# Performance work log

Hardware: AMD Instinct MI355X
Metric: run time of the kernel (lower is better)

## Reference

```python
import jax, jax.numpy as jnp
import numpy as np


def setup_inputs() -> dict:
    key = jax.random.key(0)
    k1, k2, k3, k4 = jax.random.split(key, 4)
    B, N, dim, heads, dim_head = 4, 1025, 768, 12, 64
    inner = heads * dim_head
    x = jax.random.normal(k1, (B, N, dim), dtype=jnp.float32)
    # binary occlusion mask over the N-1 patch tokens (CLS handled inside forward)
    mask = (jax.random.uniform(k2, (B, N - 1, dim)) > 0.5).astype(jnp.float32)
    w_qkv = jax.random.normal(k3, (inner * 3, dim), dtype=jnp.float32) * 0.02
    w_out = jax.random.normal(k4, (dim, inner), dtype=jnp.float32) * 0.02
    b_out = jnp.zeros((dim,), dtype=jnp.float32)
    return {"x": x, "mask": mask, "w_qkv": w_qkv, "w_out": w_out, "b_out": b_out, "heads": heads}


def reference(x, mask, w_qkv, w_out, b_out, heads):
    B, N, dim = x.shape
    inner = w_qkv.shape[0] // 3
    d = inner // heads
    scale = d ** -0.5

    def split_heads(t):  # [B, n, h*d] -> [B, h, n, d]
        return t.reshape(B, t.shape[1], heads, d).transpose(0, 2, 1, 3)

    qkv = x @ w_qkv.T  # [B, N, 3*inner]
    q, k, v = map(split_heads, jnp.split(qkv, 3, axis=-1))

    # --- mask propagation (torch.no_grad block) ---
    mask_sg = jax.lax.stop_gradient(mask)
    qkv_m = mask_sg @ jax.lax.stop_gradient(jnp.abs(w_qkv)).T  # [B, N-1, 3*inner]

    def norm_mask(t):
        t = split_heads(t)  # [B, h, N-1, d]
        t = t / (1e-6 + jnp.max(t, axis=2, keepdims=True))
        return jnp.concatenate([jnp.ones_like(t[:, :, :1]), t], axis=2)  # [B, h, N, d]

    q_m, k_m, v_m = map(norm_mask, jnp.split(qkv_m, 3, axis=-1))
    updated = (jnp.mean(mask_sg, axis=-1, keepdims=True) > 0.0).astype(x.dtype)  # [B, N-1, 1]
    updated = jnp.concatenate([jnp.ones_like(updated[:, :1]), updated], axis=1)  # [B, N, 1]

    # --- masked attention ---
    dots = jnp.einsum('bhnd,bhmd->bhnm', q * q_m, k * k_m) * scale
    attn = jax.nn.softmax(dots, axis=-1)
    out = jnp.einsum('bhnm,bhmd->bhnd', attn, v_m * v)
    out = out.transpose(0, 2, 1, 3).reshape(B, N, inner) * updated
    out = out @ w_out.T + b_out

    # --- mask output propagation (no grad) ---
    m = jax.lax.stop_gradient(jnp.einsum('bhnm,bhmd->bhnd', attn, v_m))
    m = m.transpose(0, 2, 1, 3).reshape(B, N, inner) * updated
    m = m @ jax.lax.stop_gradient(jnp.abs(w_out)).T
    return (out, m[:, 1:])
```

## Files before the change

kernel.cpp:

```cpp
#include <hip/hip_runtime.h>
#include <cmath>

#define TPB 256
#define ATPB 128

static const int NTOK  = 1025;
static const int DIM   = 768;
static const int HEADS = 12;
static const int QK3   = 2304;
static const int ROWS  = 4 * NTOK;
static const int MROWS = 4 * (NTOK - 1);
static const int MPAD  = 4224;
static const int NPAD  = 1088;
static const int VROWS = 129;
static const size_t OUT0 = (size_t)ROWS * DIM;
static const size_t APLANE = (size_t)MPAD * DIM;

static const size_t OFF_QKV16  = 0;
static const size_t OFF_QKVM16 = 4800000;
static const size_t OFF_QE     = 9600000;
static const size_t OFF_KE     = 11300000;
static const size_t OFF_VT     = 13000000;
static const size_t OFF_ABF    = 16400000;
static const size_t OFF_WQ     = 19700000;
static const size_t OFF_WO     = 21500000;
static const size_t OFF_CMAX   = 22100000;
static const size_t OFF_UPD    = 22110000;

typedef __attribute__((ext_vector_type(8))) short short8;
typedef __attribute__((ext_vector_type(4))) float f32x4;

__device__ __forceinline__ unsigned short f2bf(float f) {
    union { float f; unsigned int u; } c; c.f = f;
    unsigned int u = c.u + 0x7fffu + ((c.u >> 16) & 1u);
    return (unsigned short)(u >> 16);
}
__device__ __forceinline__ float bf2f(unsigned short u) {
    union { unsigned int u; float f; } c; c.u = (unsigned int)u << 16;
    return c.f;
}
__device__ __forceinline__ void gl_lds16(const unsigned short* g, unsigned short* l) {
    __builtin_amdgcn_global_load_lds(
        (const __attribute__((address_space(1))) unsigned int*)g,
        (__attribute__((address_space(3))) unsigned int*)l, 16, 0, 0);
}

__global__ __launch_bounds__(TPB)
void k_cvt(const float* __restrict__ x, const float* __restrict__ mask,
           const float* __restrict__ wqkv, const float* __restrict__ wout,
           unsigned short* __restrict__ Abf, unsigned short* __restrict__ Wq,
           unsigned short* __restrict__ Wo)
{
    const int z = blockIdx.z;
    const size_t idx = ((size_t)blockIdx.x * TPB + threadIdx.x) * 8;
    unsigned short o[8] __attribute__((aligned(16)));
    if (z <= 1) {
        if (idx >= APLANE) return;
        const int row = (int)(idx / DIM);
        const int M = z ? MROWS : ROWS;
        const float* src = z ? mask : x;
        if (row < M) {
            float a[8];
            *(float4*)&a[0] = *(const float4*)(src + idx);
            *(float4*)&a[4] = *(const float4*)(src + idx + 4);
#pragma unroll
            for (int i = 0; i < 8; ++i) o[i] = f2bf(a[i]);
        } else {
#pragma unroll
            for (int i = 0; i < 8; ++i) o[i] = 0;
        }
        *(short8*)(Abf + (size_t)z * APLANE + idx) = *(short8*)o;
    } else {
        const size_t tot = (z == 2) ? (size_t)QK3 * DIM : (size_t)DIM * DIM;
        if (idx >= tot) return;
        const float* src = (z == 2) ? wqkv : wout;
        unsigned short* dst = (z == 2) ? Wq : Wo;
        float a[8];
        *(float4*)&a[0] = *(const float4*)(src + idx);
        *(float4*)&a[4] = *(const float4*)(src + idx + 4);
        unsigned short oa[8] __attribute__((aligned(16)));
#pragma unroll
        for (int i = 0; i < 8; ++i) { o[i] = f2bf(a[i]); oa[i] = f2bf(fabsf(a[i])); }
        *(short8*)(dst + idx) = *(short8*)o;
        *(short8*)(dst + tot + idx) = *(short8*)oa;
    }
}

__global__ __launch_bounds__(TPB)
void k_gemm_qkv_mfma(const unsigned short* __restrict__ Abf,
                     const unsigned short* __restrict__ Wq,
                     unsigned short* __restrict__ qkv16,
                     unsigned short* __restrict__ qkvm16,
                     float* __restrict__ cmax)
{
    const int z = blockIdx.z;
    const int rowT = blockIdx.y * 128, colT = blockIdx.x * 128;
    if (z == 1 && rowT >= MROWS) return;
    const unsigned short* A = Abf + (size_t)z * APLANE;
    const unsigned short* B = Wq + (size_t)z * QK3 * DIM;

    __shared__ unsigned short As[128 * 64];
    __shared__ unsigned short Bs[128 * 64];

    const int t = threadIdx.x;
    const int w = t >> 6, lane = t & 63, l15 = lane & 15, quad = lane >> 4;
    const int wm = (w & 1) * 64, wn = (w >> 1) * 64;
    const int sr = t >> 2, sk = (t & 3) * 8;

    f32x4 acc[4][4];
#pragma unroll
    for (int i = 0; i < 4; ++i)
#pragma unroll
        for (int j = 0; j < 4; ++j) acc[i][j] = (f32x4){0.f, 0.f, 0.f, 0.f};

    for (int k0 = 0; k0 < DIM; k0 += 64) {
        __syncthreads();
#pragma unroll
        for (int c = 0; c < 4; ++c) {
            const int gr = sr + (c & 1) * 64;
            const int gk = k0 + (c >> 1) * 32 + sk;
            gl_lds16(A + (size_t)(rowT + gr) * DIM + gk, As + c * 2048 + t * 8);
            gl_lds16(B + (size_t)(colT + gr) * DIM + gk, Bs + c * 2048 + t * 8);
        }
        __syncthreads();
        short8 fa[2][4], fb[2][4];
#pragma unroll
        for (int kk = 0; kk < 2; ++kk) {
#pragma unroll
            for (int mi = 0; mi < 4; ++mi)
                fa[kk][mi] = *(const short8*)(As + kk * 4096 + (wm + mi * 16 + l15) * 32 + quad * 8);
#pragma unroll
            for (int ni = 0; ni < 4; ++ni)
                fb[kk][ni] = *(const short8*)(Bs + kk * 4096 + (wn + ni * 16 + l15) * 32 + quad * 8);
        }
#pragma unroll
        for (int kk = 0; kk < 2; ++kk)
#pragma unroll
            for (int mi = 0; mi < 4; ++mi)
#pragma unroll
                for (int ni = 0; ni < 4; ++ni)
                    acc[mi][ni] = __builtin_amdgcn_mfma_f32_16x16x32_bf16(fa[kk][mi], fb[kk][ni], acc[mi][ni], 0, 0, 0);
    }

    float cm[4] = {0.f, 0.f, 0.f, 0.f};
#pragma unroll
    for (int mi = 0; mi < 4; ++mi)
#pragma unroll
        for (int ni = 0; ni < 4; ++ni) {
            const int col = colT + wn + ni * 16 + l15;
#pragma unroll
            for (int r = 0; r < 4; ++r) {
                const int row = rowT + wm + mi * 16 + quad * 4 + r;
                const float v = acc[mi][ni][r];
                if (z == 0) {
                    if (row < ROWS) qkv16[(size_t)row * QK3 + col] = f2bf(v);
                } else {
                    qkvm16[(size_t)row * QK3 + col] = f2bf(v);
                    cm[ni] = fmaxf(cm[ni], v);
                }
            }
        }
    if (z == 1) {
        const int bb = rowT >> 10;
#pragma unroll
        for (int ni = 0; ni < 4; ++ni) {
            float m = cm[ni];
            m = fmaxf(m, __shfl_xor(m, 16, 64));
            m = fmaxf(m, __shfl_xor(m, 32, 64));
            if (quad == 0)
                atomicMax((int*)&cmax[bb * QK3 + colT + wn + ni * 16 + l15], __float_as_int(m));
        }
    }
}

__global__ __launch_bounds__(TPB)
void k_misc(const float* __restrict__ mask, float* __restrict__ upd,
            unsigned short* __restrict__ vt)
{
    const int bx = blockIdx.x;
    if (bx >= 1025) {
        const int bh = bx - 1025;
        unsigned short* p = vt + ((size_t)bh * VROWS + 128) * NPAD;
        for (int n = threadIdx.x; n < NPAD; n += TPB)
            p[n] = (n < NTOK) ? (unsigned short)0x3F80 : (unsigned short)0;
        return;
    }
    const int w = threadIdx.x >> 6, lane = threadIdx.x & 63;
    const int r = bx * 4 + w;
    if (r >= ROWS) return;
    const int b = r / NTOK, n = r % NTOK;
    float res = 1.f;
    if (n > 0) {
        const float* p = mask + (size_t)(b * (NTOK - 1) + (n - 1)) * DIM;
        float s = 0.f;
        for (int i = lane; i < DIM; i += 64) s += p[i];
#pragma unroll
        for (int off = 32; off > 0; off >>= 1) s += __shfl_xor(s, off, 64);
        res = (s > 0.f) ? 1.f : 0.f;
    }
    if (lane == 0) upd[r] = res;
}

__global__ __launch_bounds__(TPB)
void k_prep(const unsigned short* __restrict__ qkv16,
            const unsigned short* __restrict__ qkvm16,
            const float* __restrict__ cmax, unsigned short* __restrict__ qe,
            unsigned short* __restrict__ ke, unsigned short* __restrict__ vt)
{
    __shared__ unsigned short Vt_l[128 * 66];
    const int t = threadIdx.x;
    const int nt = blockIdx.x, h = blockIdx.y, b = blockIdx.z;
    const int bh = b * HEADS + h;
    const int nl = t >> 2, ds0 = (t & 3) * 16;
    const int n = nt * 64 + nl;
    const bool valid = n < NTOK;
    const int col0 = h * 64 + ds0;

    unsigned short q16[16] __attribute__((aligned(16))) = {0};
    unsigned short k16[16] __attribute__((aligned(16))) = {0};
    unsigned short v16[16] __attribute__((aligned(16))) = {0};
    unsigned short qm16[16] __attribute__((aligned(16)));
    unsigned short km16[16] __attribute__((aligned(16)));
    unsigned short vm16[16] __attribute__((aligned(16)));
    float cq[16], ck[16], cv[16];

    const bool useM = valid && (n > 0);
    if (valid) {
        const size_t br = (size_t)(b * NTOK + n) * QK3 + col0;
        *(short8*)&q16[0] = *(const short8*)(qkv16 + br);
        *(short8*)&q16[8] = *(const short8*)(qkv16 + br + 8);
        *(short8*)&k16[0] = *(const short8*)(qkv16 + br + 768);
        *(short8*)&k16[8] = *(const short8*)(qkv16 + br + 776);
        *(short8*)&v16[0] = *(const short8*)(qkv16 + br + 1536);
        *(short8*)&v16[8] = *(const short8*)(qkv16 + br + 1544);
    }
    if (useM) {
        const size_t mr = (size_t)(b * 1024 + (n - 1)) * QK3 + col0;
        *(short8*)&qm16[0] = *(const short8*)(qkvm16 + mr);
        *(short8*)&qm16[8] = *(const short8*)(qkvm16 + mr + 8);
        *(short8*)&km16[0] = *(const short8*)(qkvm16 + mr + 768);
        *(short8*)&km16[8] = *(const short8*)(qkvm16 + mr + 776);
        *(short8*)&vm16[0] = *(const short8*)(qkvm16 + mr + 1536);
        *(short8*)&vm16[8] = *(const short8*)(qkvm16 + mr + 1544);
        const int cb = b * QK3 + col0;
#pragma unroll
        for (int i = 0; i < 4; ++i) {
            *(float4*)&cq[i * 4] = *(const float4*)(cmax + cb + i * 4);
            *(float4*)&ck[i * 4] = *(const float4*)(cmax + cb + 768 + i * 4);
            *(float4*)&cv[i * 4] = *(const float4*)(cmax + cb + 1536 + i * 4);
        }
    }

    unsigned short oq[16] __attribute__((aligned(16)));
    unsigned short ok[16] __attribute__((aligned(16)));
#pragma unroll
    for (int idx = 0; idx < 16; ++idx) {
        const float qm = useM ? bf2f(qm16[idx]) / (1e-6f + cq[idx]) : 1.f;
        const float km = useM ? bf2f(km16[idx]) / (1e-6f + ck[idx]) : 1.f;
        const float vm = valid ? (useM ? bf2f(vm16[idx]) / (1e-6f + cv[idx]) : 1.f) : 0.f;
        oq[idx] = f2bf(bf2f(q16[idx]) * qm * 0.125f);
        ok[idx] = f2bf(bf2f(k16[idx]) * km);
        const int d = ds0 + idx;
        Vt_l[d * 66 + nl]        = f2bf(bf2f(v16[idx]) * vm);
        Vt_l[(64 + d) * 66 + nl] = f2bf(vm);
    }
    if (valid) {
        unsigned short* qp = qe + ((size_t)bh * NPAD + n) * 64 + ds0;
        unsigned short* kp = ke + ((size_t)bh * NPAD + n) * 64 + ds0;
        *(short8*)qp       = *(short8*)oq;
        *(short8*)(qp + 8) = *(short8*)(oq + 8);
        *(short8*)kp       = *(short8*)ok;
        *(short8*)(kp + 8) = *(short8*)(ok + 8);
    }
    __syncthreads();
    const int c = t >> 1, nh = (t & 1) * 32;
    unsigned short ov[32] __attribute__((aligned(16)));
#pragma unroll
    for (int i = 0; i < 32; ++i) ov[i] = Vt_l[c * 66 + nh + i];
    unsigned short* vp = vt + ((size_t)bh * VROWS + c) * NPAD + nt * 64 + nh;
#pragma unroll
    for (int i = 0; i < 4; ++i) *(short8*)(vp + i * 8) = *(short8*)(ov + i * 8);
}

__global__ __launch_bounds__(ATPB)
void k_attn(const unsigned short* __restrict__ qe, const unsigned short* __restrict__ ke,
            const unsigned short* __restrict__ vt, const float* __restrict__ upd,
            unsigned short* __restrict__ ab2)
{
    __shared__ short8 KsF[8 * 64];
    __shared__ short8 VsF[18 * 64];

    const int t = threadIdx.x;
    const int w = t >> 6, lane = t & 63;
    const int l15 = lane & 15, quad = lane >> 4;
    const int bh = blockIdx.y;
    const int b = bh / HEADS, h = bh % HEADS;
    const int q0 = blockIdx.x * 64;

    short8 qf[2][2];
#pragma unroll
    for (int j = 0; j < 2; ++j) {
        const unsigned short* qp = qe + ((size_t)bh * NPAD + q0 + w * 32 + j * 16 + l15) * 64 + (quad << 3);
        qf[j][0] = *(const short8*)qp;
        qf[j][1] = *(const short8*)(qp + 32);
    }
    const int pA = (quad & 1) * 32 + l15;
    const int pB = pA + 16;
    const bool lo32 = (lane < 32);

    f32x4 acc[2][9];
#pragma unroll
    for (int j = 0; j < 2; ++j)
#pragma unroll
        for (int g = 0; g < 9; ++g) acc[j][g] = (f32x4){0.f, 0.f, 0.f, 0.f};

    for (int kt = 0; kt < 17; ++kt) {
        const int kn0 = kt * 64;
        __syncthreads();
#pragma unroll
        for (int gi = 0; gi < 4; ++gi) {
            const int g = 4 * w + gi, kk = g >> 2, nc = g & 3;
            const unsigned short* gp = ke + ((size_t)bh * NPAD + kn0 + nc * 16 + l15) * 64
                                          + kk * 32 + (quad << 3);
            gl_lds16(gp, (unsigned short*)&KsF[g * 64] + lane * 8);
        }
#pragma unroll
        for (int i = 0; i < 9; ++i) {
            const int g = w + 2 * i;
            const int kk = (g >= 9) ? 1 : 0, c8 = g - kk * 9;
            const unsigned short* gp = vt + ((size_t)bh * VROWS + c8 * 16 + l15) * NPAD
                                          + kn0 + kk * 32 + (quad << 3);
            gl_lds16(gp, (unsigned short*)&VsF[g * 64] + lane * 8);
        }
        __syncthreads();

        f32x4 s[2][4];
#pragma unroll
        for (int nc = 0; nc < 4; ++nc) {
            const short8 k0 = KsF[nc * 64 + lane];
            const short8 k1 = KsF[(4 + nc) * 64 + lane];
#pragma unroll
            for (int j = 0; j < 2; ++j) {
                f32x4 z = (f32x4){0.f, 0.f, 0.f, 0.f};
                z = __builtin_amdgcn_mfma_f32_16x16x32_bf16(k0, qf[j][0], z, 0, 0, 0);
                z = __builtin_amdgcn_mfma_f32_16x16x32_bf16(k1, qf[j][1], z, 0, 0, 0);
                s[j][nc] = z;
            }
        }
        short8 pf[2][2];
#pragma unroll
        for (int j = 0; j < 2; ++j) {
            unsigned int dA[4], dB[4];
#pragma unroll
            for (int nc = 0; nc < 4; ++nc) {
                const float p0 = __expf(s[j][nc][0] - 10.f);
                const float p1 = __expf(s[j][nc][1] - 10.f);
                const float p2 = __expf(s[j][nc][2] - 10.f);
                const float p3 = __expf(s[j][nc][3] - 10.f);
                dA[nc] = (unsigned int)f2bf(p0) | ((unsigned int)f2bf(p1) << 16);
                dB[nc] = (unsigned int)f2bf(p2) | ((unsigned int)f2bf(p3) << 16);
            }
            union { int i[4]; short8 s; } u0, u1;
            {
                const int a0 = __shfl((int)dA[0], pA, 64), a1 = __shfl((int)dA[1], pA, 64);
                const int b0 = __shfl((int)dB[0], pA, 64), b1 = __shfl((int)dB[1], pA, 64);
                const int a2 = __shfl((int)dA[0], pB, 64), a3 = __shfl((int)dA[1], pB, 64);
                const int b2 = __shfl((int)dB[0], pB, 64), b3 = __shfl((int)dB[1], pB, 64);
                u0.i[0] = lo32 ? a0 : a1;
                u0.i[1] = lo32 ? b0 : b1;
                u0.i[2] = lo32 ? a2 : a3;
                u0.i[3] = lo32 ? b2 : b3;
            }
            {
                const int a0 = __shfl((int)dA[2], pA, 64), a1 = __shfl((int)dA[3], pA, 64);
                const int b0 = __shfl((int)dB[2], pA, 64), b1 = __shfl((int)dB[3], pA, 64);
                const int a2 = __shfl((int)dA[2], pB, 64), a3 = __shfl((int)dA[3], pB, 64);
                const int b2 = __shfl((int)dB[2], pB, 64), b3 = __shfl((int)dB[3], pB, 64);
                u1.i[0] = lo32 ? a0 : a1;
                u1.i[1] = lo32 ? b0 : b1;
                u1.i[2] = lo32 ? a2 : a3;
                u1.i[3] = lo32 ? b2 : b3;
            }
            pf[j][0] = u0.s;
            pf[j][1] = u1.s;
        }
#pragma unroll
        for (int g = 0; g < 9; ++g) {
            const short8 v0 = VsF[g * 64 + lane];
            const short8 v1 = VsF[(9 + g) * 64 + lane];
#pragma unroll
            for (int j = 0; j < 2; ++j) {
                acc[j][g] = __builtin_amdgcn_mfma_f32_16x16x32_bf16(v0, pf[j][0], acc[j][g], 0, 0, 0);
                acc[j][g] = __builtin_amdgcn_mfma_f32_16x16x32_bf16(v1, pf[j][1], acc[j][g], 0, 0, 0);
            }
        }
    }

#pragma unroll
    for (int j = 0; j < 2; ++j) {
        const float lq = __shfl(acc[j][8][0], l15, 64);
        const int qrow = q0 + w * 32 + j * 16 + l15;
        if (qrow < NTOK) {
            const size_t rg = (size_t)b * NTOK + qrow;
            const float inv = upd[rg] / lq;
#pragma unroll
            for (int g = 0; g < 8; ++g) {
                uint2 pk;
                pk.x = (unsigned int)f2bf(acc[j][g][0] * inv) | ((unsigned int)f2bf(acc[j][g][1] * inv) << 16);
                pk.y = (unsigned int)f2bf(acc[j][g][2] * inv) | ((unsigned int)f2bf(acc[j][g][3] * inv) << 16);
                const size_t addr = (size_t)(g >> 2) * APLANE + rg * DIM + h * 64 + (g & 3) * 16 + quad * 4;
                *(uint2*)(ab2 + addr) = pk;
            }
        }
    }
}

__global__ __launch_bounds__(TPB)
void k_gemm_out_mfma(const unsigned short* __restrict__ ab2,
                     const unsigned short* __restrict__ Wo,
                     const float* __restrict__ bout, float* __restrict__ dout)
{
    const int z = blockIdx.z;
    const unsigned short* A = ab2 + (size_t)z * APLANE;
    const unsigned short* B = Wo + (size_t)z * DIM * DIM;

    __shared__ unsigned short As[128 * 32];
    __shared__ unsigned short Bs[128 * 32];

    const int t = threadIdx.x;
    const int w = t >> 6, lane = t & 63, l15 = lane & 15, quad = lane >> 4;
    const int rowT = blockIdx.y * 128, colT = blockIdx.x * 128;
    const int wm = (w & 1) * 64, wn = (w >> 1) * 64;

    const int r0 = t >> 2, kc = (t & 3) * 8;
    const unsigned short* Ap = A + (size_t)(rowT + r0) * DIM + kc;
    const unsigned short* Bp = B + (size_t)(colT + r0) * DIM + kc;

    f32x4 acc[4][4];
#pragma unroll
    for (int i = 0; i < 4; ++i)
#pragma unroll
        for (int j = 0; j < 4; ++j) acc[i][j] = (f32x4){0.f, 0.f, 0.f, 0.f};

    for (int k0 = 0; k0 < DIM; k0 += 32) {
        __syncthreads();
        gl_lds16(Ap + k0,            As + t * 8);
        gl_lds16(Ap + 64 * DIM + k0, As + (t + 256) * 8);
        gl_lds16(Bp + k0,            Bs + t * 8);
        gl_lds16(Bp + 64 * DIM + k0, Bs + (t + 256) * 8);
        __syncthreads();
        short8 fa[4], fb[4];
#pragma unroll
        for (int mi = 0; mi < 4; ++mi)
            fa[mi] = *(const short8*)(As + (wm + mi * 16 + l15) * 32 + quad * 8);
#pragma unroll
        for (int ni = 0; ni < 4; ++ni)
            fb[ni] = *(const short8*)(Bs + (wn + ni * 16 + l15) * 32 + quad * 8);
#pragma unroll
        for (int mi = 0; mi < 4; ++mi)
#pragma unroll
            for (int ni = 0; ni < 4; ++ni)
                acc[mi][ni] = __builtin_amdgcn_mfma_f32_16x16x32_bf16(fa[mi], fb[ni], acc[mi][ni], 0, 0, 0);
    }
#pragma unroll
    for (int mi = 0; mi < 4; ++mi)
#pragma unroll
        for (int ni = 0; ni < 4; ++ni) {
            const int col = colT + wn + ni * 16 + l15;
            const float bb = (z == 0) ? bout[col] : 0.f;
#pragma unroll
            for (int r = 0; r < 4; ++r) {
                const int row = rowT + wm + mi * 16 + quad * 4 + r;
                if (row >= ROWS) continue;
                const int b = row / NTOK, n = row % NTOK;
                if (z == 0) {
                    dout[(size_t)row * DIM + col] = acc[mi][ni][r] + bb;
                } else if (n >= 1) {
                    dout[OUT0 + ((size_t)(b * (NTOK - 1) + (n - 1))) * DIM + col] = acc[mi][ni][r];
                }
            }
        }
}

extern "C" void kernel_launch(void* const* d_in, const int* in_sizes, int n_in,
                              void* d_out, int out_size, void* d_ws, size_t ws_size,
                              hipStream_t stream)
{
    const float* x    = (const float*)d_in[0];
    const float* mask = (const float*)d_in[1];
    const float* wqkv = (const float*)d_in[2];
    const float* wout = (const float*)d_in[3];
    const float* bout = (const float*)d_in[4];
    float* ws = (float*)d_ws;
    unsigned short* qkv16  = (unsigned short*)(ws + OFF_QKV16);
    unsigned short* qkvm16 = (unsigned short*)(ws + OFF_QKVM16);
    unsigned short* qe  = (unsigned short*)(ws + OFF_QE);
    unsigned short* ke  = (unsigned short*)(ws + OFF_KE);
    unsigned short* vt  = (unsigned short*)(ws + OFF_VT);
    unsigned short* abf = (unsigned short*)(ws + OFF_ABF);
    unsigned short* wq  = (unsigned short*)(ws + OFF_WQ);
    unsigned short* wo  = (unsigned short*)(ws + OFF_WO);
    float* cmax = ws + OFF_CMAX;
    float* upd  = ws + OFF_UPD;
    float* out  = (float*)d_out;

    hipMemsetAsync(cmax, 0, 9216 * sizeof(float), stream);
    hipLaunchKernelGGL(k_cvt,           dim3(1584, 1, 4), dim3(TPB), 0, stream, x, mask, wqkv, wout, abf, wq, wo);
    hipLaunchKernelGGL(k_gemm_qkv_mfma, dim3(18, 33, 2),  dim3(TPB), 0, stream, abf, wq, qkv16, qkvm16, cmax);
    hipLaunchKernelGGL(k_misc,          dim3(1073),       dim3(TPB), 0, stream, mask, upd, vt);
    hipLaunchKernelGGL(k_prep,          dim3(17, 12, 4),  dim3(TPB), 0, stream, qkv16, qkvm16, cmax, qe, ke, vt);
    hipLaunchKernelGGL(k_attn,          dim3(17, 48),     dim3(ATPB), 0, stream, qe, ke, vt, upd, abf);
    hipLaunchKernelGGL(k_gemm_out_mfma, dim3(6, 33, 2),   dim3(TPB), 0, stream, abf, wo, bout, out);
}
```

Before: 249.0 us.

## Store K/V in MFMA fragment layout and load directly into registers in attention

The prep kernel now writes K and V directly in MFMA fragment order, so the attention kernel can load K/V tiles straight into registers instead of staging them through LDS behind barriers. Attention becomes one 64-thread wave per 32-query tile with a swizzled block order and register prefetch of the next K/V tile. The softmax denominator is now accumulated in registers rather than through an extra ones-row in V, which removes the 129th row and its memset pass. Exponentials switch to exp2 with log2e folded into the Q scale, bf16 packing uses v_cvt_pk_bf16_f32, and s_setprio is raised around the MFMA sections. In exchange the kernel carries more register pressure from the prefetched fragments, and LDS reuse of K/V across waves is lost.

```diff
diff --git a/kernel.cpp b/kernel.cpp
--- a/kernel.cpp
+++ b/kernel.cpp
@@ -2,7 +2,6 @@
 #include <cmath>
 
 #define TPB 256
-#define ATPB 128
 
 static const int NTOK  = 1025;
 static const int DIM   = 768;
@@ -12,15 +11,14 @@
 static const int MROWS = 4 * (NTOK - 1);
 static const int MPAD  = 4224;
 static const int NPAD  = 1088;
-static const int VROWS = 129;
 static const size_t OUT0 = (size_t)ROWS * DIM;
 static const size_t APLANE = (size_t)MPAD * DIM;
 
 static const size_t OFF_QKV16  = 0;
 static const size_t OFF_QKVM16 = 4800000;
 static const size_t OFF_QE     = 9600000;
-static const size_t OFF_KE     = 11300000;
-static const size_t OFF_VT     = 13000000;
+static const size_t OFF_KF     = 11300000;
+static const size_t OFF_VF     = 13000000;
 static const size_t OFF_ABF    = 16400000;
 static const size_t OFF_WQ     = 19700000;
 static const size_t OFF_WO     = 21500000;
@@ -38,6 +36,11 @@
 __device__ __forceinline__ float bf2f(unsigned short u) {
     union { unsigned int u; float f; } c; c.u = (unsigned int)u << 16;
     return c.f;
+}
+__device__ __forceinline__ unsigned int cvtpk(float a, float b) {
+    unsigned int r;
+    asm("v_cvt_pk_bf16_f32 %0, %1, %2" : "=v"(r) : "v"(a), "v"(b));
+    return r;
 }
 __device__ __forceinline__ void gl_lds16(const unsigned short* g, unsigned short* l) {
     __builtin_amdgcn_global_load_lds(
@@ -174,17 +177,9 @@
 }
 
 __global__ __launch_bounds__(TPB)
-void k_misc(const float* __restrict__ mask, float* __restrict__ upd,
-            unsigned short* __restrict__ vt)
+void k_misc(const float* __restrict__ mask, float* __restrict__ upd)
 {
     const int bx = blockIdx.x;
-    if (bx >= 1025) {
-        const int bh = bx - 1025;
-        unsigned short* p = vt + ((size_t)bh * VROWS + 128) * NPAD;
-        for (int n = threadIdx.x; n < NPAD; n += TPB)
-            p[n] = (n < NTOK) ? (unsigned short)0x3F80 : (unsigned short)0;
-        return;
-    }
     const int w = threadIdx.x >> 6, lane = threadIdx.x & 63;
     const int r = bx * 4 + w;
     if (r >= ROWS) return;
@@ -205,7 +200,7 @@
 void k_prep(const unsigned short* __restrict__ qkv16,
             const unsigned short* __restrict__ qkvm16,
             const float* __restrict__ cmax, unsigned short* __restrict__ qe,
-            unsigned short* __restrict__ ke, unsigned short* __restrict__ vt)
+            unsigned short* __restrict__ kfrag, unsigned short* __restrict__ vfrag)
 {
     __shared__ unsigned short Vt_l[128 * 66];
     const int t = threadIdx.x;
@@ -258,49 +253,53 @@
         const float qm = useM ? bf2f(qm16[idx]) / (1e-6f + cq[idx]) : 1.f;
         const float km = useM ? bf2f(km16[idx]) / (1e-6f + ck[idx]) : 1.f;
         const float vm = valid ? (useM ? bf2f(vm16[idx]) / (1e-6f + cv[idx]) : 1.f) : 0.f;
-        oq[idx] = f2bf(bf2f(q16[idx]) * qm * 0.125f);
+        oq[idx] = f2bf(bf2f(q16[idx]) * qm * 0.18033688f);
         ok[idx] = f2bf(bf2f(k16[idx]) * km);
         const int d = ds0 + idx;
         Vt_l[d * 66 + nl]        = f2bf(bf2f(v16[idx]) * vm);
         Vt_l[(64 + d) * 66 + nl] = f2bf(vm);
     }
-    if (valid) {
+    {
         unsigned short* qp = qe + ((size_t)bh * NPAD + n) * 64 + ds0;
-        unsigned short* kp = ke + ((size_t)bh * NPAD + n) * 64 + ds0;
         *(short8*)qp       = *(short8*)oq;
         *(short8*)(qp + 8) = *(short8*)(oq + 8);
-        *(short8*)kp       = *(short8*)ok;
-        *(short8*)(kp + 8) = *(short8*)(ok + 8);
+    }
+    {
+        const int nc = nl >> 4, l15 = nl & 15;
+        const int kk = ds0 >> 5, qb = (ds0 & 31) >> 3;
+        unsigned short* kp = kfrag + (((size_t)bh * 17 + nt) * 8 + kk * 4 + nc) * 512;
+        *(short8*)(kp + ((size_t)(qb * 16 + l15)) * 8)       = *(short8*)ok;
+        *(short8*)(kp + ((size_t)((qb + 1) * 16 + l15)) * 8) = *(short8*)(ok + 8);
     }
     __syncthreads();
     const int c = t >> 1, nh = (t & 1) * 32;
     unsigned short ov[32] __attribute__((aligned(16)));
 #pragma unroll
     for (int i = 0; i < 32; ++i) ov[i] = Vt_l[c * 66 + nh + i];
-    unsigned short* vp = vt + ((size_t)bh * VROWS + c) * NPAD + nt * 64 + nh;
-#pragma unroll
-    for (int i = 0; i < 4; ++i) *(short8*)(vp + i * 8) = *(short8*)(ov + i * 8);
-}
-
-__global__ __launch_bounds__(ATPB)
-void k_attn(const unsigned short* __restrict__ qe, const unsigned short* __restrict__ ke,
-            const unsigned short* __restrict__ vt, const float* __restrict__ upd,
+    const int c8 = c >> 4, l15v = c & 15, kkv = nh >> 5;
+    unsigned short* vp = vfrag + (((size_t)bh * 17 + nt) * 16 + c8 * 2 + kkv) * 512 + (size_t)l15v * 8;
+#pragma unroll
+    for (int qd = 0; qd < 4; ++qd)
+        *(short8*)(vp + (size_t)qd * 128) = *(short8*)(ov + qd * 8);
+}
+
+__global__ __launch_bounds__(64, 2)
+void k_attn(const unsigned short* __restrict__ qe, const unsigned short* __restrict__ kfrag,
+            const unsigned short* __restrict__ vfrag, const float* __restrict__ upd,
             unsigned short* __restrict__ ab2)
 {
-    __shared__ short8 KsF[8 * 64];
-    __shared__ short8 VsF[18 * 64];
-
-    const int t = threadIdx.x;
-    const int w = t >> 6, lane = t & 63;
+    const int flat = blockIdx.y * 33 + blockIdx.x;
+    const int d2 = (flat & 7) * 198 + (flat >> 3);
+    const int bh = d2 / 33, qt = d2 - bh * 33;
+    const int b = bh / HEADS, h = bh - b * HEADS;
+    const int lane = threadIdx.x;
     const int l15 = lane & 15, quad = lane >> 4;
-    const int bh = blockIdx.y;
-    const int b = bh / HEADS, h = bh % HEADS;
-    const int q0 = blockIdx.x * 64;
+    const int q0 = qt * 32;
 
     short8 qf[2][2];
 #pragma unroll
     for (int j = 0; j < 2; ++j) {
-        const unsigned short* qp = qe + ((size_t)bh * NPAD + q0 + w * 32 + j * 16 + l15) * 64 + (quad << 3);
+        const unsigned short* qp = qe + ((size_t)bh * NPAD + q0 + j * 16 + l15) * 64 + (quad << 3);
         qf[j][0] = *(const short8*)qp;
         qf[j][1] = *(const short8*)(qp + 32);
     }
@@ -308,58 +307,62 @@
     const int pB = pA + 16;
     const bool lo32 = (lane < 32);
 
-    f32x4 acc[2][9];
+    const unsigned short* kb = kfrag + (size_t)bh * (17 * 8 * 512) + (size_t)lane * 8;
+    const unsigned short* vb = vfrag + (size_t)bh * (17 * 16 * 512) + (size_t)lane * 8;
+
+    short8 kf[8], vf[16];
+#pragma unroll
+    for (int g = 0; g < 8; ++g) kf[g] = *(const short8*)(kb + g * 512);
+#pragma unroll
+    for (int g = 0; g < 16; ++g) vf[g] = *(const short8*)(vb + g * 512);
+
+    f32x4 acc[2][8];
+    float lac[2] = {0.f, 0.f};
 #pragma unroll
     for (int j = 0; j < 2; ++j)
 #pragma unroll
-        for (int g = 0; g < 9; ++g) acc[j][g] = (f32x4){0.f, 0.f, 0.f, 0.f};
-
+        for (int g = 0; g < 8; ++g) acc[j][g] = (f32x4){0.f, 0.f, 0.f, 0.f};
+
+    const float EC = 14.4269504f;
+
+#pragma clang loop unroll(disable)
     for (int kt = 0; kt < 17; ++kt) {
-        const int kn0 = kt * 64;
-        __syncthreads();
-#pragma unroll
-        for (int gi = 0; gi < 4; ++gi) {
-            const int g = 4 * w + gi, kk = g >> 2, nc = g & 3;
-            const unsigned short* gp = ke + ((size_t)bh * NPAD + kn0 + nc * 16 + l15) * 64
-                                          + kk * 32 + (quad << 3);
-            gl_lds16(gp, (unsigned short*)&KsF[g * 64] + lane * 8);
-        }
-#pragma unroll
-        for (int i = 0; i < 9; ++i) {
-            const int g = w + 2 * i;
-            const int kk = (g >= 9) ? 1 : 0, c8 = g - kk * 9;
-            const unsigned short* gp = vt + ((size_t)bh * VROWS + c8 * 16 + l15) * NPAD
-                                          + kn0 + kk * 32 + (quad << 3);
-            gl_lds16(gp, (unsigned short*)&VsF[g * 64] + lane * 8);
-        }
-        __syncthreads();
-
         f32x4 s[2][4];
+        __builtin_amdgcn_s_setprio(1);
 #pragma unroll
         for (int nc = 0; nc < 4; ++nc) {
-            const short8 k0 = KsF[nc * 64 + lane];
-            const short8 k1 = KsF[(4 + nc) * 64 + lane];
 #pragma unroll
             for (int j = 0; j < 2; ++j) {
                 f32x4 z = (f32x4){0.f, 0.f, 0.f, 0.f};
-                z = __builtin_amdgcn_mfma_f32_16x16x32_bf16(k0, qf[j][0], z, 0, 0, 0);
-                z = __builtin_amdgcn_mfma_f32_16x16x32_bf16(k1, qf[j][1], z, 0, 0, 0);
+                z = __builtin_amdgcn_mfma_f32_16x16x32_bf16(kf[nc], qf[j][0], z, 0, 0, 0);
+                z = __builtin_amdgcn_mfma_f32_16x16x32_bf16(kf[4 + nc], qf[j][1], z, 0, 0, 0);
                 s[j][nc] = z;
             }
+        }
+        __builtin_amdgcn_s_setprio(0);
+        if (kt < 16) {
+            const unsigned short* kn = kb + (size_t)(kt + 1) * 4096;
+#pragma unroll
+            for (int g = 0; g < 8; ++g) kf[g] = *(const short8*)(kn + g * 512);
         }
         short8 pf[2][2];
 #pragma unroll
         for (int j = 0; j < 2; ++j) {
             unsigned int dA[4], dB[4];
+            float psum = 0.f, p00 = 0.f;
 #pragma unroll
             for (int nc = 0; nc < 4; ++nc) {
-                const float p0 = __expf(s[j][nc][0] - 10.f);
-                const float p1 = __expf(s[j][nc][1] - 10.f);
-                const float p2 = __expf(s[j][nc][2] - 10.f);
-                const float p3 = __expf(s[j][nc][3] - 10.f);
-                dA[nc] = (unsigned int)f2bf(p0) | ((unsigned int)f2bf(p1) << 16);
-                dB[nc] = (unsigned int)f2bf(p2) | ((unsigned int)f2bf(p3) << 16);
-            }
+                const float p0 = __builtin_amdgcn_exp2f(s[j][nc][0] - EC);
+                const float p1 = __builtin_amdgcn_exp2f(s[j][nc][1] - EC);
+                const float p2 = __builtin_amdgcn_exp2f(s[j][nc][2] - EC);
+                const float p3 = __builtin_amdgcn_exp2f(s[j][nc][3] - EC);
+                dA[nc] = cvtpk(p0, p1);
+                dB[nc] = cvtpk(p2, p3);
+                psum += (p0 + p1) + (p2 + p3);
+                if (nc == 0) p00 = p0;
+            }
+            if (kt < 16) lac[j] += psum;
+            else if (quad == 0) lac[j] += p00;
             union { int i[4]; short8 s; } u0, u1;
             {
                 const int a0 = __shfl((int)dA[0], pA, 64), a1 = __shfl((int)dA[1], pA, 64);
@@ -384,30 +387,37 @@
             pf[j][0] = u0.s;
             pf[j][1] = u1.s;
         }
-#pragma unroll
-        for (int g = 0; g < 9; ++g) {
-            const short8 v0 = VsF[g * 64 + lane];
-            const short8 v1 = VsF[(9 + g) * 64 + lane];
+        __builtin_amdgcn_s_setprio(1);
+#pragma unroll
+        for (int g = 0; g < 8; ++g) {
 #pragma unroll
             for (int j = 0; j < 2; ++j) {
-                acc[j][g] = __builtin_amdgcn_mfma_f32_16x16x32_bf16(v0, pf[j][0], acc[j][g], 0, 0, 0);
-                acc[j][g] = __builtin_amdgcn_mfma_f32_16x16x32_bf16(v1, pf[j][1], acc[j][g], 0, 0, 0);
-            }
+                acc[j][g] = __builtin_amdgcn_mfma_f32_16x16x32_bf16(vf[2 * g],     pf[j][0], acc[j][g], 0, 0, 0);
+                acc[j][g] = __builtin_amdgcn_mfma_f32_16x16x32_bf16(vf[2 * g + 1], pf[j][1], acc[j][g], 0, 0, 0);
+            }
+        }
+        __builtin_amdgcn_s_setprio(0);
+        if (kt < 16) {
+            const unsigned short* vn = vb + (size_t)(kt + 1) * 8192;
+#pragma unroll
+            for (int g = 0; g < 16; ++g) vf[g] = *(const short8*)(vn + g * 512);
         }
     }
 
 #pragma unroll
     for (int j = 0; j < 2; ++j) {
-        const float lq = __shfl(acc[j][8][0], l15, 64);
-        const int qrow = q0 + w * 32 + j * 16 + l15;
+        float lq = lac[j];
+        lq += __shfl_xor(lq, 16, 64);
+        lq += __shfl_xor(lq, 32, 64);
+        const int qrow = q0 + j * 16 + l15;
         if (qrow < NTOK) {
             const size_t rg = (size_t)b * NTOK + qrow;
             const float inv = upd[rg] / lq;
 #pragma unroll
             for (int g = 0; g < 8; ++g) {
                 uint2 pk;
-                pk.x = (unsigned int)f2bf(acc[j][g][0] * inv) | ((unsigned int)f2bf(acc[j][g][1] * inv) << 16);
-                pk.y = (unsigned int)f2bf(acc[j][g][2] * inv) | ((unsigned int)f2bf(acc[j][g][3] * inv) << 16);
+                pk.x = cvtpk(acc[j][g][0] * inv, acc[j][g][1] * inv);
+                pk.y = cvtpk(acc[j][g][2] * inv, acc[j][g][3] * inv);
                 const size_t addr = (size_t)(g >> 2) * APLANE + rg * DIM + h * 64 + (g & 3) * 16 + quad * 4;
                 *(uint2*)(ab2 + addr) = pk;
             }
@@ -495,8 +505,8 @@
     unsigned short* qkv16  = (unsigned short*)(ws + OFF_QKV16);
     unsigned short* qkvm16 = (unsigned short*)(ws + OFF_QKVM16);
     unsigned short* qe  = (unsigned short*)(ws + OFF_QE);
-    unsigned short* ke  = (unsigned short*)(ws + OFF_KE);
-    unsigned short* vt  = (unsigned short*)(ws + OFF_VT);
+    unsigned short* kfr = (unsigned short*)(ws + OFF_KF);
+    unsigned short* vfr = (unsigned short*)(ws + OFF_VF);
     unsigned short* abf = (unsigned short*)(ws + OFF_ABF);
     unsigned short* wq  = (unsigned short*)(ws + OFF_WQ);
     unsigned short* wo  = (unsigned short*)(ws + OFF_WO);
@@ -507,8 +517,8 @@
     hipMemsetAsync(cmax, 0, 9216 * sizeof(float), stream);
     hipLaunchKernelGGL(k_cvt,           dim3(1584, 1, 4), dim3(TPB), 0, stream, x, mask, wqkv, wout, abf, wq, wo);
     hipLaunchKernelGGL(k_gemm_qkv_mfma, dim3(18, 33, 2),  dim3(TPB), 0, stream, abf, wq, qkv16, qkvm16, cmax);
-    hipLaunchKernelGGL(k_misc,          dim3(1073),       dim3(TPB), 0, stream, mask, upd, vt);
-    hipLaunchKernelGGL(k_prep,          dim3(17, 12, 4),  dim3(TPB), 0, stream, qkv16, qkvm16, cmax, qe, ke, vt);
-    hipLaunchKernelGGL(k_attn,          dim3(17, 48),     dim3(ATPB), 0, stream, qe, ke, vt, upd, abf);
+    hipLaunchKernelGGL(k_misc,          dim3(1025),       dim3(TPB), 0, stream, mask, upd);
+    hipLaunchKernelGGL(k_prep,          dim3(17, 12, 4),  dim3(TPB), 0, stream, qkv16, qkvm16, cmax, qe, kfr, vfr);
+    hipLaunchKernelGGL(k_attn,          dim3(33, 48),     dim3(64),  0, stream, qe, kfr, vfr, upd, abf);
     hipLaunchKernelGGL(k_gemm_out_mfma, dim3(6, 33, 2),   dim3(TPB), 0, stream, abf, wo, bout, out);
 }
```

Result: faster. 220.7 us (-11.4%).
